# Kernel optimization log

Hardware: AMD Instinct MI355X
Metric: run time of the kernel (lower is better)

The kernel has to match this reference:

```python
import jax, jax.numpy as jnp
import numpy as np

DIM = 1024
N_HEADS = 16
HEAD_DIM = DIM // N_HEADS
HIDDEN = 4 * DIM
B, T = 4, 2048
EPS = 1e-5


def setup_inputs() -> dict:
    key = jax.random.key(0)
    ks = jax.random.split(key, 12)
    s = lambda fan_in: 1.0 / np.sqrt(fan_in)
    return {
        "x": jax.random.normal(ks[0], (B, T, DIM), jnp.float32),
        "ln1_g": jnp.ones((DIM,), jnp.float32),
        "ln1_b": jnp.zeros((DIM,), jnp.float32),
        "qkv_w": jax.random.normal(ks[1], (DIM, 3 * DIM), jnp.float32) * s(DIM),
        "qkv_b": jnp.zeros((3 * DIM,), jnp.float32),
        "proj_w": jax.random.normal(ks[2], (DIM, DIM), jnp.float32) * s(DIM),
        "proj_b": jnp.zeros((DIM,), jnp.float32),
        "ln2_g": jnp.ones((DIM,), jnp.float32),
        "ln2_b": jnp.zeros((DIM,), jnp.float32),
        "ff1_w": jax.random.normal(ks[3], (DIM, HIDDEN), jnp.float32) * s(DIM),
        "ff1_b": jnp.zeros((HIDDEN,), jnp.float32),
        "ff2_w": jax.random.normal(ks[4], (HIDDEN, DIM), jnp.float32) * s(HIDDEN),
        "ff2_b": jnp.zeros((DIM,), jnp.float32),
    }


def _layernorm(x, g, b):
    mu = jnp.mean(x, axis=-1, keepdims=True)
    var = jnp.mean(jnp.square(x - mu), axis=-1, keepdims=True)
    return (x - mu) * jax.lax.rsqrt(var + EPS) * g + b


def _attn(x, qkv_w, qkv_b, proj_w, proj_b):
    Bx, Tx, C = x.shape
    qkv = (x @ qkv_w + qkv_b).reshape(Bx, Tx, 3, N_HEADS, HEAD_DIM)
    q, k, v = (qkv[:, :, i].transpose(0, 2, 1, 3) for i in range(3))  # [B,H,T,hd]
    att = jnp.einsum('bhqd,bhkd->bhqk', q, k) / np.sqrt(HEAD_DIM)
    causal = jnp.tril(jnp.ones((Tx, Tx), bool))
    att = jnp.where(causal, att, -jnp.inf)
    att = jax.nn.softmax(att, axis=-1)
    out = jnp.einsum('bhqk,bhkd->bhqd', att, v).transpose(0, 2, 1, 3).reshape(Bx, Tx, C)
    return out @ proj_w + proj_b


def reference(x, ln1_g, ln1_b, qkv_w, qkv_b, proj_w, proj_b,
              ln2_g, ln2_b, ff1_w, ff1_b, ff2_w, ff2_b):
    x = x + _attn(_layernorm(x, ln1_g, ln1_b), qkv_w, qkv_b, proj_w, proj_b)
    h = _layernorm(x, ln2_g, ln2_b)
    h = jax.nn.gelu(h @ ff1_w + ff1_b, approximate=False) @ ff2_w + ff2_b
    return x + h
```

## Files before the change

### kernel.cpp

```cpp
#include <hip/hip_runtime.h>
#include <hip/hip_bf16.h>
#include <math.h>

#define DIM 1024
#define NHEADS 16
#define HD 64
#define TT 2048
#define BB 4
#define MTOK (BB*TT)
#define HID 4096

typedef __attribute__((ext_vector_type(8))) short bf16x8;
typedef __attribute__((ext_vector_type(4))) float f32x4;
typedef unsigned short u16;
typedef unsigned int u32;

__device__ inline u16 f2b(float f){
  __hip_bfloat16 h = __float2bfloat16(f);
  return __builtin_bit_cast(u16, h);
}

__device__ inline u32 cvtpk(float lo, float hi_){
  u32 r;
  asm("v_cvt_pk_bf16_f32 %0, %1, %2" : "=v"(r) : "v"(lo), "v"(hi_));
  return r;
}

__device__ inline void load_lds16(const void* g, void* l){
  __builtin_amdgcn_global_load_lds(
      (const __attribute__((address_space(1))) void*)g,
      (__attribute__((address_space(3))) void*)l,
      16, 0, 0);
}

__global__ __launch_bounds__(256) void wconv_t(const float* __restrict__ W,
                                               u16* __restrict__ Wt, int K, int N){
  __shared__ float tl[32][33];
  const int k0 = blockIdx.x*32, n0 = blockIdx.y*32;
  const int tx = threadIdx.x & 31, ty = threadIdx.x >> 5;
  #pragma unroll
  for (int r=0;r<32;r+=8)
    tl[ty+r][tx] = W[(size_t)(k0+ty+r)*N + (n0+tx)];
  __syncthreads();
  #pragma unroll
  for (int r=0;r<32;r+=8)
    Wt[(size_t)(n0+ty+r)*K + (k0+tx)] = f2b(tl[tx][ty+r]);
}

__global__ __launch_bounds__(256) void ln_fwd(const float* __restrict__ x,
                                              const float* __restrict__ g,
                                              const float* __restrict__ bta,
                                              u16* __restrict__ out){
  const int row = blockIdx.x, t = threadIdx.x;
  const float4 v = ((const float4*)(x + (size_t)row*DIM))[t];
  float s  = v.x+v.y+v.z+v.w;
  float s2 = v.x*v.x+v.y*v.y+v.z*v.z+v.w*v.w;
  #pragma unroll
  for (int m=1;m<64;m<<=1){ s += __shfl_xor(s,m); s2 += __shfl_xor(s2,m); }
  __shared__ float red[8];
  if ((t&63)==0){ red[t>>6]=s; red[4+(t>>6)]=s2; }
  __syncthreads();
  s  = red[0]+red[1]+red[2]+red[3];
  s2 = red[4]+red[5]+red[6]+red[7];
  const float mu = s*(1.0f/DIM);
  const float rstd = rsqrtf(s2*(1.0f/DIM) - mu*mu + 1e-5f);
  const float4 gv = ((const float4*)g)[t];
  const float4 bv = ((const float4*)bta)[t];
  ushort4 ov;
  ov.x = f2b((v.x-mu)*rstd*gv.x + bv.x);
  ov.y = f2b((v.y-mu)*rstd*gv.y + bv.y);
  ov.z = f2b((v.z-mu)*rstd*gv.z + bv.z);
  ov.w = f2b((v.w-mu)*rstd*gv.w + bv.w);
  ((ushort4*)out)[(size_t)row*(DIM/4) + t] = ov;
}

template<int EPI>
__global__ __launch_bounds__(256) void gemm_bt(
    const u16* __restrict__ A, const u16* __restrict__ Bt,
    const float* __restrict__ bias, const float* __restrict__ resid,
    float* __restrict__ outf, u16* __restrict__ outh,
    u16* __restrict__ qo, u16* __restrict__ ko, u16* __restrict__ vo,
    int M, int N, int K)
{
  __shared__ __align__(16) u16 smem[16384];
  u16* As = smem;
  u16* Bs = smem + 8192;
  u16* Ct = smem;
  const int t = threadIdx.x, wv = t>>6, ln = t&63;
  const int nbx = gridDim.x, nwg = nbx*gridDim.y;
  const int bid = blockIdx.y*nbx + blockIdx.x;
  const int cpx = nwg>>3;
  const int wid = (bid&7)*cpx + (bid>>3);
  const int m0 = (wid/nbx)*128, n0 = (wid%nbx)*128;
  const int wr = wv>>1, wc = wv&1;
  const int hi = ln>>4, lr = hi*4, lc = ln&15;
  f32x4 acc[4][4] = {};

  int rdoff[2];
  #pragma unroll
  for (int kk=0; kk<2; kk++)
    rdoff[kk] = ((kk*4 + hi) ^ (lc&7)) << 3;

  for (int kt=0; kt<K; kt+=64){
    #pragma unroll
    for (int j=0;j<4;j++){
      const int chunk = j*256 + t;
      const int row = chunk>>3;
      const int cS  = (chunk&7) ^ (row&7);
      load_lds16(A  + (size_t)(m0+row)*K + kt + cS*8, (char*)As + chunk*16);
      load_lds16(Bt + (size_t)(n0+row)*K + kt + cS*8, (char*)Bs + chunk*16);
    }
    asm volatile("s_waitcnt vmcnt(0)" ::: "memory");
    __syncthreads();
    bf16x8 af[4][2], bfr[4][2];
    #pragma unroll
    for (int mi=0;mi<4;mi++){
      const int rbase = (wr*64 + mi*16 + lc) << 6;
      af[mi][0] = *(const bf16x8*)&As[rbase + rdoff[0]];
      af[mi][1] = *(const bf16x8*)&As[rbase + rdoff[1]];
    }
    #pragma unroll
    for (int ni=0;ni<4;ni++){
      const int rbase = (wc*64 + ni*16 + lc) << 6;
      bfr[ni][0] = *(const bf16x8*)&Bs[rbase + rdoff[0]];
      bfr[ni][1] = *(const bf16x8*)&Bs[rbase + rdoff[1]];
    }
    #pragma unroll
    for (int kk=0;kk<2;kk++)
      #pragma unroll
      for (int mi=0;mi<4;mi++)
        #pragma unroll
        for (int ni=0;ni<4;ni++)
          acc[mi][ni] = __builtin_amdgcn_mfma_f32_16x16x32_bf16(af[mi][kk], bfr[ni][kk], acc[mi][ni], 0,0,0);
    __syncthreads();
  }

  if constexpr (EPI==1 || EPI==3){
    #pragma unroll
    for (int ni=0;ni<4;ni++){
      const int gn = n0 + wc*64 + ni*16 + lc;
      const float bv = bias[gn];
      #pragma unroll
      for (int mi=0;mi<4;mi++){
        const int gmb = m0 + wr*64 + mi*16 + lr;
        f32x4 a = acc[mi][ni];
        #pragma unroll
        for (int i=0;i<4;i++){
          const size_t idx = (size_t)(gmb+i)*DIM + gn;
          outf[idx] = a[i] + bv + resid[idx];
        }
      }
    }
  } else {
    const int part = (EPI==0) ? (n0>>10) : 0;
    __syncthreads();
    #pragma unroll
    for (int ni=0;ni<4;ni++){
      const int gn = n0 + wc*64 + ni*16 + lc;
      const float bv = bias[gn];
      const int cl = wc*64 + ni*16 + lc;
      #pragma unroll
      for (int mi=0;mi<4;mi++){
        f32x4 a = acc[mi][ni];
        #pragma unroll
        for (int i=0;i<4;i++){
          const int rl = wr*64 + mi*16 + lr + i;
          float val = a[i] + bv;
          if constexpr (EPI==2){
            const float xx = val*val;
            const float w  = val * fmaf(xx, 0.10294322f, 2.30220781f);
            const float y  = exp2f(w);
            const float r_ = __builtin_amdgcn_rcpf(1.0f + y);
            val = val - val*r_;
          }
          int r = rl, c = cl;
          if (EPI==0 && part==2){ r = cl; c = rl; }
          const int chunk = c>>3;
          const int csw = (chunk&8) | ((chunk ^ (r&7)) & 7);
          Ct[(r<<7) + (csw<<3) + (c&7)] = f2b(val);
        }
      }
    }
    __syncthreads();
    const int cid = t & 7, rsub = t >> 3;
    const int bb = m0>>11, tok0b = m0&2047;
    const int h0 = (EPI==0) ? ((n0&1023)>>6) : 0;
    #pragma unroll
    for (int pass=0; pass<4; ++pass){
      const int rr = pass*32 + rsub;
      #pragma unroll
      for (int hh=0; hh<2; ++hh){
        const int chunk = hh*8 + cid;
        const int sw = (chunk&8) | ((chunk ^ (rr&7)) & 7);
        const bf16x8 vvv = *(const bf16x8*)&Ct[(rr<<7) + (sw<<3)];
        if constexpr (EPI==2){
          *(bf16x8*)&outh[(size_t)(m0+rr)*HID + n0 + chunk*8] = vvv;
        } else {
          if (part==2){
            const int head = h0 + (rr>>6), d = rr&63;
            *(bf16x8*)&vo[(((size_t)bb*NHEADS + head)*HD + d)*TT + tok0b + chunk*8] = vvv;
          } else {
            u16* dst = part ? ko : qo;
            const int head = h0 + hh;
            *(bf16x8*)&dst[(((size_t)bb*NHEADS + head)*TT + tok0b + rr)*HD + cid*8] = vvv;
          }
        }
      }
    }
  }
}

__global__ __launch_bounds__(512) void attn_fwd(
    const u16* __restrict__ qpt, const u16* __restrict__ kb, const u16* __restrict__ vtb,
    u16* __restrict__ o)
{
  __shared__ __align__(16) u16 Kd[2][64*64];
  __shared__ __align__(16) u16 Vd[2][64*64];
  const int t = threadIdx.x, wv = t>>6, ln = t&63;
  const int bid  = blockIdx.y*gridDim.x + blockIdx.x;
  const int orig = (bid&7)*128 + (bid>>3);
  const int bh   = orig>>4;
  const int qb   = 15 - (orig&15);
  const size_t base = (size_t)bh*TT*HD;
  const int hi = ln>>4, lc = ln&15;
  const int nt = 2*qb + 2;
  const int qbase = qb*128 + wv*16;
  const int qrow  = qbase + lc;

  const bf16x8 qf0 = *(const bf16x8*)(qpt + base + (size_t)qrow*HD + hi*8);
  const bf16x8 qf1 = *(const bf16x8*)(qpt + base + (size_t)qrow*HD + 32 + hi*8);
  f32x4 oacc[4] = {};
  f32x4 lsum = {0.f,0.f,0.f,0.f};
  float mrun = -1e30f;
  const float SCQ = 0.125f * 1.44269504f;
  bf16x8 ones;
  #pragma unroll
  for (int j=0;j<8;j++) ones[j] = (short)0x3F80;

  const int srow = t>>3;
  const int sch  = t&7;
  const int gch  = (sch ^ (srow&7))<<3;

  auto STAGE = [&](int nb, int kt){
    load_lds16(kb  + base + (size_t)(kt*64+srow)*HD + gch, &Kd[nb][srow*64 + sch*8]);
    load_lds16(vtb + base + (size_t)srow*TT + kt*64 + gch, &Vd[nb][srow*64 + sch*8]);
  };
  auto FRAG = [&](const u16* buf, int r, int ch)->bf16x8{
    return *(const bf16x8*)(buf + r*64 + ((ch ^ (r&7))<<3));
  };
  const int src0 = ((ln&16)<<1) + lc;
  const int src1 = src0 + 16;
  auto pick = [&](u32 w0, u32 w1, int src)->u32{
    const u32 a = (u32)__shfl((int)w0, src);
    const u32 b = (u32)__shfl((int)w1, src);
    return (hi<2) ? a : b;
  };

  int cur = 0;
  STAGE(0, 0);
  asm volatile("s_waitcnt vmcnt(0)" ::: "memory");
  __syncthreads();

  for (int kt=0; kt<nt; kt++){
    if (kt+1 < nt) STAGE(cur^1, kt+1);
    const u16* Kb = Kd[cur];
    const u16* Vb = Vd[cur];
    if (kt*64 <= qbase + 15){
      float sv[4][4];
      __builtin_amdgcn_s_setprio(1);
      #pragma unroll
      for (int cf=0;cf<4;cf++){
        const int r = cf*16 + lc;
        const bf16x8 kf0 = FRAG(Kb, r, hi);
        const bf16x8 kf1 = FRAG(Kb, r, hi+4);
        f32x4 z = {0.f,0.f,0.f,0.f};
        z = __builtin_amdgcn_mfma_f32_16x16x32_bf16(kf0, qf0, z, 0,0,0);
        z = __builtin_amdgcn_mfma_f32_16x16x32_bf16(kf1, qf1, z, 0,0,0);
        sv[cf][0]=z[0]; sv[cf][1]=z[1]; sv[cf][2]=z[2]; sv[cf][3]=z[3];
      }
      __builtin_amdgcn_s_setprio(0);
      float mx = -1e30f;
      if (kt*64 + 63 > qbase){
        #pragma unroll
        for (int cf=0;cf<4;cf++)
          #pragma unroll
          for (int i=0;i<4;i++){
            const int kvg = kt*64 + cf*16 + 4*hi + i;
            float s_ = sv[cf][i]*SCQ;
            s_ = (kvg > qrow) ? -1e30f : s_;
            sv[cf][i] = s_;
            mx = fmaxf(mx, s_);
          }
      } else {
        #pragma unroll
        for (int cf=0;cf<4;cf++)
          #pragma unroll
          for (int i=0;i<4;i++){
            const float s_ = sv[cf][i]*SCQ;
            sv[cf][i] = s_;
            mx = fmaxf(mx, s_);
          }
      }
      mx = fmaxf(mx, __shfl_xor(mx, 16));
      mx = fmaxf(mx, __shfl_xor(mx, 32));
      if (__any(mx > mrun + 11.0f)){
        const float mnew = fmaxf(mrun, mx);
        const float sc = exp2f(mrun - mnew);
        mrun = mnew;
        const float s0 = __shfl(sc, 4*hi+0);
        const float s1 = __shfl(sc, 4*hi+1);
        const float s2 = __shfl(sc, 4*hi+2);
        const float s3 = __shfl(sc, 4*hi+3);
        #pragma unroll
        for (int df=0;df<4;df++){
          oacc[df][0] *= s0; oacc[df][1] *= s1;
          oacc[df][2] *= s2; oacc[df][3] *= s3;
        }
        lsum[0] *= s0; lsum[1] *= s1; lsum[2] *= s2; lsum[3] *= s3;
      }
      u32 W[4][2];
      #pragma unroll
      for (int cf=0;cf<4;cf++){
        const float e0 = exp2f(sv[cf][0] - mrun);
        const float e1 = exp2f(sv[cf][1] - mrun);
        const float e2 = exp2f(sv[cf][2] - mrun);
        const float e3 = exp2f(sv[cf][3] - mrun);
        W[cf][0] = cvtpk(e0, e1);
        W[cf][1] = cvtpk(e2, e3);
      }
      uint4 uA, uB;
      uA.x = pick(W[0][0], W[1][0], src0);
      uA.y = pick(W[0][1], W[1][1], src0);
      uA.z = pick(W[0][0], W[1][0], src1);
      uA.w = pick(W[0][1], W[1][1], src1);
      uB.x = pick(W[2][0], W[3][0], src0);
      uB.y = pick(W[2][1], W[3][1], src0);
      uB.z = pick(W[2][0], W[3][0], src1);
      uB.w = pick(W[2][1], W[3][1], src1);
      const bf16x8 paA = __builtin_bit_cast(bf16x8, uA);
      const bf16x8 paB = __builtin_bit_cast(bf16x8, uB);
      __builtin_amdgcn_s_setprio(1);
      #pragma unroll
      for (int df=0;df<4;df++){
        const bf16x8 v0 = FRAG(Vb, df*16+lc, hi);
        const bf16x8 v1 = FRAG(Vb, df*16+lc, hi+4);
        oacc[df] = __builtin_amdgcn_mfma_f32_16x16x32_bf16(paA, v0, oacc[df], 0,0,0);
        oacc[df] = __builtin_amdgcn_mfma_f32_16x16x32_bf16(paB, v1, oacc[df], 0,0,0);
      }
      lsum = __builtin_amdgcn_mfma_f32_16x16x32_bf16(paA, ones, lsum, 0,0,0);
      lsum = __builtin_amdgcn_mfma_f32_16x16x32_bf16(paB, ones, lsum, 0,0,0);
      __builtin_amdgcn_s_setprio(0);
    }
    asm volatile("s_waitcnt vmcnt(0)" ::: "memory");
    __syncthreads();
    cur ^= 1;
  }

  const int b = bh>>4, h = bh&15;
  const float inv[4] = {1.0f/lsum[0], 1.0f/lsum[1], 1.0f/lsum[2], 1.0f/lsum[3]};
  const int qg0 = qbase + 4*hi;
  #pragma unroll
  for (int i=0;i<4;i++){
    const size_t rowb = ((size_t)b*TT + (size_t)(qg0 + i))*DIM + h*HD;
    #pragma unroll
    for (int df=0;df<4;df++)
      o[rowb + df*16 + lc] = f2b(oacc[df][i]*inv[i]);
  }
}

extern "C" void kernel_launch(void* const* d_in, const int* in_sizes, int n_in,
                              void* d_out, int out_size, void* d_ws, size_t ws_size,
                              hipStream_t stream){
  (void)in_sizes; (void)n_in; (void)out_size; (void)ws_size;
  const float* x     = (const float*)d_in[0];
  const float* ln1g  = (const float*)d_in[1];
  const float* ln1b  = (const float*)d_in[2];
  const float* qkvw  = (const float*)d_in[3];
  const float* qkvb  = (const float*)d_in[4];
  const float* projw = (const float*)d_in[5];
  const float* projb = (const float*)d_in[6];
  const float* ln2g  = (const float*)d_in[7];
  const float* ln2b  = (const float*)d_in[8];
  const float* ff1w  = (const float*)d_in[9];
  const float* ff1b  = (const float*)d_in[10];
  const float* ff2w  = (const float*)d_in[11];
  const float* ff2b  = (const float*)d_in[12];
  float* out = (float*)d_out;

  char* ws = (char*)d_ws;
  size_t off = 0;
  auto alloc = [&](size_t n){ char* p = ws + off; off += (n + 255) & ~(size_t)255; return p; };
  u16* wqkvt  = (u16*)alloc((size_t)3072*1024*2);
  u16* wprojt = (u16*)alloc((size_t)1024*1024*2);
  u16* wff1t  = (u16*)alloc((size_t)4096*1024*2);
  u16* wff2t  = (u16*)alloc((size_t)1024*4096*2);
  u16* h1     = (u16*)alloc((size_t)MTOK*DIM*2);
  u16* qbuf   = (u16*)alloc((size_t)MTOK*DIM*2);
  u16* kbuf   = (u16*)alloc((size_t)MTOK*DIM*2);
  u16* vbuf   = (u16*)alloc((size_t)MTOK*DIM*2);
  u16* aout   = (u16*)alloc((size_t)MTOK*DIM*2);
  float* x2   = (float*)alloc((size_t)MTOK*DIM*4);
  u16* h2     = (u16*)alloc((size_t)MTOK*DIM*2);
  u16* act    = (u16*)alloc((size_t)MTOK*HID*2);

  wconv_t<<<dim3(1024/32, 3072/32), 256, 0, stream>>>(qkvw, wqkvt, 1024, 3072);
  wconv_t<<<dim3(1024/32, 1024/32), 256, 0, stream>>>(projw, wprojt, 1024, 1024);
  wconv_t<<<dim3(1024/32, 4096/32), 256, 0, stream>>>(ff1w, wff1t, 1024, 4096);
  wconv_t<<<dim3(4096/32, 1024/32), 256, 0, stream>>>(ff2w, wff2t, 4096, 1024);

  ln_fwd<<<MTOK, 256, 0, stream>>>(x, ln1g, ln1b, h1);

  gemm_bt<0><<<dim3(3072/128, MTOK/128), 256, 0, stream>>>(
      h1, wqkvt, qkvb, nullptr, nullptr, nullptr, qbuf, kbuf, vbuf, MTOK, 3072, 1024);

  attn_fwd<<<dim3(TT/128, BB*NHEADS), 512, 0, stream>>>(qbuf, kbuf, vbuf, aout);

  gemm_bt<1><<<dim3(1024/128, MTOK/128), 256, 0, stream>>>(
      aout, wprojt, projb, x, x2, nullptr, nullptr, nullptr, nullptr, MTOK, 1024, 1024);

  ln_fwd<<<MTOK, 256, 0, stream>>>(x2, ln2g, ln2b, h2);

  gemm_bt<2><<<dim3(4096/128, MTOK/128), 256, 0, stream>>>(
      h2, wff1t, ff1b, nullptr, nullptr, act, nullptr, nullptr, nullptr, MTOK, HID, 1024);

  gemm_bt<3><<<dim3(1024/128, MTOK/128), 256, 0, stream>>>(
      act, wff2t, ff2b, x2, out, nullptr, nullptr, nullptr, nullptr, MTOK, DIM, HID);
}
```

Measured before the change: 464.2 us.

## Add 256x256-tile double-buffered GEMM for QKV and FF1 projections

Introduces a new 512-thread GEMM kernel with 256x256 output tiles, 128KB of dynamic LDS, a double-buffered K pipeline that interleaves global-to-LDS staging with MFMA work, and an LDS-staged epilogue for the QKV scatter and the GELU output. It is used for the QKV and FF1 GEMMs when the large shared-memory attribute can be set, and falls back to the old kernel otherwise. The larger tiles raise arithmetic intensity and cut redundant operand loads. In exchange the grid has fewer workgroups, so occupancy is lower, and register pressure rises from the 8x4 accumulator array per wave.

```diff
diff --git a/kernel.cpp b/kernel.cpp
--- a/kernel.cpp
+++ b/kernel.cpp
@@ -72,6 +72,148 @@
   ov.z = f2b((v.z-mu)*rstd*gv.z + bv.z);
   ov.w = f2b((v.w-mu)*rstd*gv.w + bv.w);
   ((ushort4*)out)[(size_t)row*(DIM/4) + t] = ov;
+}
+
+template<int EPI>
+__global__ __launch_bounds__(512, 2) void gemm256(
+    const u16* __restrict__ A, const u16* __restrict__ Bt,
+    const float* __restrict__ bias, u16* __restrict__ outh,
+    u16* __restrict__ qo, u16* __restrict__ ko, u16* __restrict__ vo,
+    int K)
+{
+  extern __shared__ __align__(16) u16 smem[];
+  u16* Ct = smem;
+  const int t = threadIdx.x, wv = t>>6, ln = t&63;
+  const int nbx = gridDim.x, nwg = nbx*gridDim.y;
+  const int bid = blockIdx.y*nbx + blockIdx.x;
+  const int cpx = nwg>>3;
+  const int wid = (bid&7)*cpx + (bid>>3);
+  const int m0 = (wid/nbx)*256, n0 = (wid%nbx)*256;
+  const int wr = wv>>2, wc = wv&3;
+  const int hi = ln>>4, lc = ln&15;
+  f32x4 acc[8][4] = {};
+
+  auto STAGE = [&](int buf, int kt, int which, int kk){
+    const u16* src = which ? Bt : A;
+    const int org = which ? n0 : m0;
+    u16* dst = smem + buf*32768 + which*16384 + kk*8192;
+    #pragma unroll
+    for (int j=0;j<2;j++){
+      const int id = j*512 + t;
+      const int row = id>>2, c = id&3;
+      load_lds16(src + (size_t)(org+row)*K + kt*64 + kk*32 + ((c^(row&3))<<3),
+                 (char*)(dst + id*8));
+    }
+  };
+  auto AFRAG = [&](int buf, int kk, int r)->bf16x8{
+    return *(const bf16x8*)(smem + buf*32768 + kk*8192 + r*32 + ((hi^(r&3))<<3));
+  };
+  auto BFRAG = [&](int buf, int kk, int r)->bf16x8{
+    return *(const bf16x8*)(smem + buf*32768 + 16384 + kk*8192 + r*32 + ((hi^(r&3))<<3));
+  };
+
+  const int nkt = K>>6;
+  STAGE(0,0,0,0); STAGE(0,0,1,0); STAGE(0,0,0,1); STAGE(0,0,1,1);
+  asm volatile("s_waitcnt vmcnt(4)" ::: "memory");
+  __builtin_amdgcn_s_barrier();
+
+  int cur = 0;
+  for (int tt=0; tt<nkt; ++tt){
+    const int nxt = cur^1;
+    const bool st = (tt+1) < nkt;
+    bf16x8 bfr[4];
+    #pragma unroll
+    for (int p=0;p<4;p++){
+      const int kk = p>>1, mh = p&1;
+      if (mh==0){
+        #pragma unroll
+        for (int ni=0;ni<4;ni++)
+          bfr[ni] = BFRAG(cur, kk, wc*64 + ni*16 + lc);
+      }
+      bf16x8 af[4];
+      #pragma unroll
+      for (int mi=0;mi<4;mi++)
+        af[mi] = AFRAG(cur, kk, wr*128 + (mh*4+mi)*16 + lc);
+      if (st) STAGE(nxt, tt+1, p&1, p>>1);
+      __builtin_amdgcn_s_setprio(1);
+      #pragma unroll
+      for (int mi=0;mi<4;mi++)
+        #pragma unroll
+        for (int ni=0;ni<4;ni++)
+          acc[mh*4+mi][ni] = __builtin_amdgcn_mfma_f32_16x16x32_bf16(af[mi], bfr[ni], acc[mh*4+mi][ni], 0,0,0);
+      __builtin_amdgcn_s_setprio(0);
+      if (p==1 || p==3){
+        if (st) asm volatile("s_waitcnt vmcnt(4)" ::: "memory");
+        else    asm volatile("s_waitcnt vmcnt(0)" ::: "memory");
+        __builtin_amdgcn_s_barrier();
+      }
+    }
+    cur = nxt;
+  }
+
+  const int bb = m0>>11;
+  #pragma unroll
+  for (int h=0;h<2;h++){
+    #pragma unroll
+    for (int ch=0;ch<2;ch++){
+      const int part = (EPI==0) ? ((n0 + ch*128)>>10) : 0;
+      const int h0 = ((n0 + ch*128)&1023)>>6;
+      __syncthreads();
+      if (wr==h && (wc>>1)==ch){
+        #pragma unroll
+        for (int ni=0;ni<4;ni++){
+          const int gn = n0 + wc*64 + ni*16 + lc;
+          const float bv = bias[gn];
+          const int cl = (wc&1)*64 + ni*16 + lc;
+          #pragma unroll
+          for (int mi=0;mi<8;mi++){
+            f32x4 a = acc[mi][ni];
+            #pragma unroll
+            for (int i=0;i<4;i++){
+              const int rl = mi*16 + hi*4 + i;
+              float val = a[i] + bv;
+              if constexpr (EPI==2){
+                const float xx = val*val;
+                const float w  = val * fmaf(xx, 0.10294322f, 2.30220781f);
+                const float y  = exp2f(w);
+                const float r_ = __builtin_amdgcn_rcpf(1.0f + y);
+                val = val - val*r_;
+              }
+              int r = rl, c = cl;
+              if (EPI==0 && part==2){ r = cl; c = rl; }
+              const int chunk = c>>3;
+              const int csw = (chunk&8) | ((chunk ^ (r&7)) & 7);
+              Ct[(r<<7) + (csw<<3) + (c&7)] = f2b(val);
+            }
+          }
+        }
+      }
+      __syncthreads();
+      const int cid = t&7, rsub = t>>3;
+      const int tok0b = (m0&2047) + h*128;
+      #pragma unroll
+      for (int p2=0;p2<2;p2++){
+        const int rr = p2*64 + rsub;
+        #pragma unroll
+        for (int hh=0;hh<2;hh++){
+          const int chunk = hh*8 + cid;
+          const int sw = (chunk&8) | ((chunk ^ (rr&7)) & 7);
+          const bf16x8 vvv = *(const bf16x8*)&Ct[(rr<<7) + (sw<<3)];
+          if constexpr (EPI==2){
+            *(bf16x8*)&outh[(size_t)(m0 + h*128 + rr)*HID + n0 + ch*128 + chunk*8] = vvv;
+          } else {
+            if (part==2){
+              const int head = h0 + (rr>>6), d = rr&63;
+              *(bf16x8*)&vo[(((size_t)bb*NHEADS + head)*HD + d)*TT + tok0b + chunk*8] = vvv;
+            } else {
+              u16* dst = part ? ko : qo;
+              *(bf16x8*)&dst[(((size_t)bb*NHEADS + h0 + hh)*TT + tok0b + rr)*HD + cid*8] = vvv;
+            }
+          }
+        }
+      }
+    }
+  }
 }
 
 template<int EPI>
@@ -403,6 +545,12 @@
   u16* h2     = (u16*)alloc((size_t)MTOK*DIM*2);
   u16* act    = (u16*)alloc((size_t)MTOK*HID*2);
 
+  hipError_t eA = hipFuncSetAttribute(reinterpret_cast<const void*>(&gemm256<0>),
+                                      hipFuncAttributeMaxDynamicSharedMemorySize, 131072);
+  hipError_t eB = hipFuncSetAttribute(reinterpret_cast<const void*>(&gemm256<2>),
+                                      hipFuncAttributeMaxDynamicSharedMemorySize, 131072);
+  const bool big = (eA == hipSuccess) && (eB == hipSuccess);
+
   wconv_t<<<dim3(1024/32, 3072/32), 256, 0, stream>>>(qkvw, wqkvt, 1024, 3072);
   wconv_t<<<dim3(1024/32, 1024/32), 256, 0, stream>>>(projw, wprojt, 1024, 1024);
   wconv_t<<<dim3(1024/32, 4096/32), 256, 0, stream>>>(ff1w, wff1t, 1024, 4096);
@@ -410,8 +558,12 @@
 
   ln_fwd<<<MTOK, 256, 0, stream>>>(x, ln1g, ln1b, h1);
 
-  gemm_bt<0><<<dim3(3072/128, MTOK/128), 256, 0, stream>>>(
-      h1, wqkvt, qkvb, nullptr, nullptr, nullptr, qbuf, kbuf, vbuf, MTOK, 3072, 1024);
+  if (big)
+    gemm256<0><<<dim3(3072/256, MTOK/256), 512, 131072, stream>>>(
+        h1, wqkvt, qkvb, nullptr, qbuf, kbuf, vbuf, 1024);
+  else
+    gemm_bt<0><<<dim3(3072/128, MTOK/128), 256, 0, stream>>>(
+        h1, wqkvt, qkvb, nullptr, nullptr, nullptr, qbuf, kbuf, vbuf, MTOK, 3072, 1024);
 
   attn_fwd<<<dim3(TT/128, BB*NHEADS), 512, 0, stream>>>(qbuf, kbuf, vbuf, aout);
 
@@ -420,8 +572,12 @@
 
   ln_fwd<<<MTOK, 256, 0, stream>>>(x2, ln2g, ln2b, h2);
 
-  gemm_bt<2><<<dim3(4096/128, MTOK/128), 256, 0, stream>>>(
-      h2, wff1t, ff1b, nullptr, nullptr, act, nullptr, nullptr, nullptr, MTOK, HID, 1024);
+  if (big)
+    gemm256<2><<<dim3(4096/256, MTOK/256), 512, 131072, stream>>>(
+        h2, wff1t, ff1b, act, nullptr, nullptr, nullptr, 1024);
+  else
+    gemm_bt<2><<<dim3(4096/128, MTOK/128), 256, 0, stream>>>(
+        h2, wff1t, ff1b, nullptr, nullptr, act, nullptr, nullptr, nullptr, MTOK, HID, 1024);
 
   gemm_bt<3><<<dim3(1024/128, MTOK/128), 256, 0, stream>>>(
       act, wff2t, ff2b, x2, out, nullptr, nullptr, nullptr, nullptr, MTOK, DIM, HID);
```

Result: slower. 514.7 us (+10.9%).

## Pair complementary causal query blocks per attention workgroup to balance work

Applied to the files above, without the earlier changes.

Each attention workgroup now processes two query blocks, qp and 15-qp, over a single shared K/V stream. The goal is to balance causal work across workgroups and reuse each staged K/V tile for both query strips. In exchange the grid halves to 512 workgroups and register pressure roughly doubles because two sets of accumulators are live, which may lower occupancy.

```diff
diff --git a/kernel.cpp b/kernel.cpp
--- a/kernel.cpp
+++ b/kernel.cpp
@@ -218,20 +218,23 @@
   __shared__ __align__(16) u16 Vd[2][64*64];
   const int t = threadIdx.x, wv = t>>6, ln = t&63;
   const int bid  = blockIdx.y*gridDim.x + blockIdx.x;
-  const int orig = (bid&7)*128 + (bid>>3);
-  const int bh   = orig>>4;
-  const int qb   = 15 - (orig&15);
+  const int orig = (bid&7)*64 + (bid>>3);
+  const int bh   = orig>>3;
+  const int qp   = orig&7;
+  const int qbA  = qp, qbB = 15-qp;
   const size_t base = (size_t)bh*TT*HD;
   const int hi = ln>>4, lc = ln&15;
-  const int nt = 2*qb + 2;
-  const int qbase = qb*128 + wv*16;
-  const int qrow  = qbase + lc;
-
-  const bf16x8 qf0 = *(const bf16x8*)(qpt + base + (size_t)qrow*HD + hi*8);
-  const bf16x8 qf1 = *(const bf16x8*)(qpt + base + (size_t)qrow*HD + 32 + hi*8);
-  f32x4 oacc[4] = {};
-  f32x4 lsum = {0.f,0.f,0.f,0.f};
-  float mrun = -1e30f;
+  const int ntA = 2*qbA + 2, ntB = 2*qbB + 2;
+  const int qbaseA = qbA*128 + wv*16, qrowA = qbaseA + lc;
+  const int qbaseB = qbB*128 + wv*16, qrowB = qbaseB + lc;
+
+  const bf16x8 qfA0 = *(const bf16x8*)(qpt + base + (size_t)qrowA*HD + hi*8);
+  const bf16x8 qfA1 = *(const bf16x8*)(qpt + base + (size_t)qrowA*HD + 32 + hi*8);
+  const bf16x8 qfB0 = *(const bf16x8*)(qpt + base + (size_t)qrowB*HD + hi*8);
+  const bf16x8 qfB1 = *(const bf16x8*)(qpt + base + (size_t)qrowB*HD + 32 + hi*8);
+  f32x4 oaccA[4] = {}, oaccB[4] = {};
+  f32x4 lsumA = {0.f,0.f,0.f,0.f}, lsumB = {0.f,0.f,0.f,0.f};
+  float mrunA = -1e30f, mrunB = -1e30f;
   const float SCQ = 0.125f * 1.44269504f;
   bf16x8 ones;
   #pragma unroll
@@ -256,115 +259,136 @@
     return (hi<2) ? a : b;
   };
 
+  auto strip_tile = [&](int kt, const u16* Kb, const u16* Vb,
+                        const bf16x8& qf0, const bf16x8& qf1,
+                        int qbase, int qrow,
+                        f32x4* oacc, f32x4& lsum, float& mrun){
+    if (kt*64 > qbase + 15) return;
+    float sv[4][4];
+    __builtin_amdgcn_s_setprio(1);
+    #pragma unroll
+    for (int cf=0;cf<4;cf++){
+      const int r = cf*16 + lc;
+      const bf16x8 kf0 = FRAG(Kb, r, hi);
+      const bf16x8 kf1 = FRAG(Kb, r, hi+4);
+      f32x4 z = {0.f,0.f,0.f,0.f};
+      z = __builtin_amdgcn_mfma_f32_16x16x32_bf16(kf0, qf0, z, 0,0,0);
+      z = __builtin_amdgcn_mfma_f32_16x16x32_bf16(kf1, qf1, z, 0,0,0);
+      sv[cf][0]=z[0]; sv[cf][1]=z[1]; sv[cf][2]=z[2]; sv[cf][3]=z[3];
+    }
+    __builtin_amdgcn_s_setprio(0);
+    float mx = -1e30f;
+    if (kt*64 + 63 > qbase){
+      #pragma unroll
+      for (int cf=0;cf<4;cf++)
+        #pragma unroll
+        for (int i=0;i<4;i++){
+          const int kvg = kt*64 + cf*16 + 4*hi + i;
+          float s_ = sv[cf][i]*SCQ;
+          s_ = (kvg > qrow) ? -1e30f : s_;
+          sv[cf][i] = s_;
+          mx = fmaxf(mx, s_);
+        }
+    } else {
+      #pragma unroll
+      for (int cf=0;cf<4;cf++)
+        #pragma unroll
+        for (int i=0;i<4;i++){
+          const float s_ = sv[cf][i]*SCQ;
+          sv[cf][i] = s_;
+          mx = fmaxf(mx, s_);
+        }
+    }
+    mx = fmaxf(mx, __shfl_xor(mx, 16));
+    mx = fmaxf(mx, __shfl_xor(mx, 32));
+    if (__any(mx > mrun + 11.0f)){
+      const float mnew = fmaxf(mrun, mx);
+      const float sc = exp2f(mrun - mnew);
+      mrun = mnew;
+      const float s0 = __shfl(sc, 4*hi+0);
+      const float s1 = __shfl(sc, 4*hi+1);
+      const float s2 = __shfl(sc, 4*hi+2);
+      const float s3 = __shfl(sc, 4*hi+3);
+      #pragma unroll
+      for (int df=0;df<4;df++){
+        oacc[df][0] *= s0; oacc[df][1] *= s1;
+        oacc[df][2] *= s2; oacc[df][3] *= s3;
+      }
+      lsum[0] *= s0; lsum[1] *= s1; lsum[2] *= s2; lsum[3] *= s3;
+    }
+    u32 W[4][2];
+    #pragma unroll
+    for (int cf=0;cf<4;cf++){
+      const float e0 = exp2f(sv[cf][0] - mrun);
+      const float e1 = exp2f(sv[cf][1] - mrun);
+      const float e2 = exp2f(sv[cf][2] - mrun);
+      const float e3 = exp2f(sv[cf][3] - mrun);
+      W[cf][0] = cvtpk(e0, e1);
+      W[cf][1] = cvtpk(e2, e3);
+    }
+    uint4 uA, uB;
+    uA.x = pick(W[0][0], W[1][0], src0);
+    uA.y = pick(W[0][1], W[1][1], src0);
+    uA.z = pick(W[0][0], W[1][0], src1);
+    uA.w = pick(W[0][1], W[1][1], src1);
+    uB.x = pick(W[2][0], W[3][0], src0);
+    uB.y = pick(W[2][1], W[3][1], src0);
+    uB.z = pick(W[2][0], W[3][0], src1);
+    uB.w = pick(W[2][1], W[3][1], src1);
+    const bf16x8 paA = __builtin_bit_cast(bf16x8, uA);
+    const bf16x8 paB = __builtin_bit_cast(bf16x8, uB);
+    __builtin_amdgcn_s_setprio(1);
+    #pragma unroll
+    for (int df=0;df<4;df++){
+      const bf16x8 v0 = FRAG(Vb, df*16+lc, hi);
+      const bf16x8 v1 = FRAG(Vb, df*16+lc, hi+4);
+      oacc[df] = __builtin_amdgcn_mfma_f32_16x16x32_bf16(paA, v0, oacc[df], 0,0,0);
+      oacc[df] = __builtin_amdgcn_mfma_f32_16x16x32_bf16(paB, v1, oacc[df], 0,0,0);
+    }
+    lsum = __builtin_amdgcn_mfma_f32_16x16x32_bf16(paA, ones, lsum, 0,0,0);
+    lsum = __builtin_amdgcn_mfma_f32_16x16x32_bf16(paB, ones, lsum, 0,0,0);
+    __builtin_amdgcn_s_setprio(0);
+  };
+
   int cur = 0;
   STAGE(0, 0);
   asm volatile("s_waitcnt vmcnt(0)" ::: "memory");
   __syncthreads();
 
-  for (int kt=0; kt<nt; kt++){
-    if (kt+1 < nt) STAGE(cur^1, kt+1);
+  for (int kt=0; kt<ntB; kt++){
+    if (kt+1 < ntB) STAGE(cur^1, kt+1);
     const u16* Kb = Kd[cur];
     const u16* Vb = Vd[cur];
-    if (kt*64 <= qbase + 15){
-      float sv[4][4];
-      __builtin_amdgcn_s_setprio(1);
-      #pragma unroll
-      for (int cf=0;cf<4;cf++){
-        const int r = cf*16 + lc;
-        const bf16x8 kf0 = FRAG(Kb, r, hi);
-        const bf16x8 kf1 = FRAG(Kb, r, hi+4);
-        f32x4 z = {0.f,0.f,0.f,0.f};
-        z = __builtin_amdgcn_mfma_f32_16x16x32_bf16(kf0, qf0, z, 0,0,0);
-        z = __builtin_amdgcn_mfma_f32_16x16x32_bf16(kf1, qf1, z, 0,0,0);
-        sv[cf][0]=z[0]; sv[cf][1]=z[1]; sv[cf][2]=z[2]; sv[cf][3]=z[3];
-      }
-      __builtin_amdgcn_s_setprio(0);
-      float mx = -1e30f;
-      if (kt*64 + 63 > qbase){
-        #pragma unroll
-        for (int cf=0;cf<4;cf++)
-          #pragma unroll
-          for (int i=0;i<4;i++){
-            const int kvg = kt*64 + cf*16 + 4*hi + i;
-            float s_ = sv[cf][i]*SCQ;
-            s_ = (kvg > qrow) ? -1e30f : s_;
-            sv[cf][i] = s_;
-            mx = fmaxf(mx, s_);
-          }
-      } else {
-        #pragma unroll
-        for (int cf=0;cf<4;cf++)
-          #pragma unroll
-          for (int i=0;i<4;i++){
-            const float s_ = sv[cf][i]*SCQ;
-            sv[cf][i] = s_;
-            mx = fmaxf(mx, s_);
-          }
-      }
-      mx = fmaxf(mx, __shfl_xor(mx, 16));
-      mx = fmaxf(mx, __shfl_xor(mx, 32));
-      if (__any(mx > mrun + 11.0f)){
-        const float mnew = fmaxf(mrun, mx);
-        const float sc = exp2f(mrun - mnew);
-        mrun = mnew;
-        const float s0 = __shfl(sc, 4*hi+0);
-        const float s1 = __shfl(sc, 4*hi+1);
-        const float s2 = __shfl(sc, 4*hi+2);
-        const float s3 = __shfl(sc, 4*hi+3);
-        #pragma unroll
-        for (int df=0;df<4;df++){
-          oacc[df][0] *= s0; oacc[df][1] *= s1;
-          oacc[df][2] *= s2; oacc[df][3] *= s3;
-        }
-        lsum[0] *= s0; lsum[1] *= s1; lsum[2] *= s2; lsum[3] *= s3;
-      }
-      u32 W[4][2];
-      #pragma unroll
-      for (int cf=0;cf<4;cf++){
-        const float e0 = exp2f(sv[cf][0] - mrun);
-        const float e1 = exp2f(sv[cf][1] - mrun);
-        const float e2 = exp2f(sv[cf][2] - mrun);
-        const float e3 = exp2f(sv[cf][3] - mrun);
-        W[cf][0] = cvtpk(e0, e1);
-        W[cf][1] = cvtpk(e2, e3);
-      }
-      uint4 uA, uB;
-      uA.x = pick(W[0][0], W[1][0], src0);
-      uA.y = pick(W[0][1], W[1][1], src0);
-      uA.z = pick(W[0][0], W[1][0], src1);
-      uA.w = pick(W[0][1], W[1][1], src1);
-      uB.x = pick(W[2][0], W[3][0], src0);
-      uB.y = pick(W[2][1], W[3][1], src0);
-      uB.z = pick(W[2][0], W[3][0], src1);
-      uB.w = pick(W[2][1], W[3][1], src1);
-      const bf16x8 paA = __builtin_bit_cast(bf16x8, uA);
-      const bf16x8 paB = __builtin_bit_cast(bf16x8, uB);
-      __builtin_amdgcn_s_setprio(1);
-      #pragma unroll
-      for (int df=0;df<4;df++){
-        const bf16x8 v0 = FRAG(Vb, df*16+lc, hi);
-        const bf16x8 v1 = FRAG(Vb, df*16+lc, hi+4);
-        oacc[df] = __builtin_amdgcn_mfma_f32_16x16x32_bf16(paA, v0, oacc[df], 0,0,0);
-        oacc[df] = __builtin_amdgcn_mfma_f32_16x16x32_bf16(paB, v1, oacc[df], 0,0,0);
-      }
-      lsum = __builtin_amdgcn_mfma_f32_16x16x32_bf16(paA, ones, lsum, 0,0,0);
-      lsum = __builtin_amdgcn_mfma_f32_16x16x32_bf16(paB, ones, lsum, 0,0,0);
-      __builtin_amdgcn_s_setprio(0);
-    }
+    strip_tile(kt, Kb, Vb, qfB0, qfB1, qbaseB, qrowB, oaccB, lsumB, mrunB);
+    if (kt < ntA)
+      strip_tile(kt, Kb, Vb, qfA0, qfA1, qbaseA, qrowA, oaccA, lsumA, mrunA);
     asm volatile("s_waitcnt vmcnt(0)" ::: "memory");
     __syncthreads();
     cur ^= 1;
   }
 
   const int b = bh>>4, h = bh&15;
-  const float inv[4] = {1.0f/lsum[0], 1.0f/lsum[1], 1.0f/lsum[2], 1.0f/lsum[3]};
-  const int qg0 = qbase + 4*hi;
-  #pragma unroll
-  for (int i=0;i<4;i++){
-    const size_t rowb = ((size_t)b*TT + (size_t)(qg0 + i))*DIM + h*HD;
-    #pragma unroll
-    for (int df=0;df<4;df++)
-      o[rowb + df*16 + lc] = f2b(oacc[df][i]*inv[i]);
+  {
+    const float inv[4] = {1.0f/lsumA[0], 1.0f/lsumA[1], 1.0f/lsumA[2], 1.0f/lsumA[3]};
+    const int qg0 = qbaseA + 4*hi;
+    #pragma unroll
+    for (int i=0;i<4;i++){
+      const size_t rowb = ((size_t)b*TT + (size_t)(qg0 + i))*DIM + h*HD;
+      #pragma unroll
+      for (int df=0;df<4;df++)
+        o[rowb + df*16 + lc] = f2b(oaccA[df][i]*inv[i]);
+    }
+  }
+  {
+    const float inv[4] = {1.0f/lsumB[0], 1.0f/lsumB[1], 1.0f/lsumB[2], 1.0f/lsumB[3]};
+    const int qg0 = qbaseB + 4*hi;
+    #pragma unroll
+    for (int i=0;i<4;i++){
+      const size_t rowb = ((size_t)b*TT + (size_t)(qg0 + i))*DIM + h*HD;
+      #pragma unroll
+      for (int df=0;df<4;df++)
+        o[rowb + df*16 + lc] = f2b(oaccB[df][i]*inv[i]);
+    }
   }
 }
 
@@ -413,7 +437,7 @@
   gemm_bt<0><<<dim3(3072/128, MTOK/128), 256, 0, stream>>>(
       h1, wqkvt, qkvb, nullptr, nullptr, nullptr, qbuf, kbuf, vbuf, MTOK, 3072, 1024);
 
-  attn_fwd<<<dim3(TT/128, BB*NHEADS), 512, 0, stream>>>(qbuf, kbuf, vbuf, aout);
+  attn_fwd<<<dim3(8, BB*NHEADS), 512, 0, stream>>>(qbuf, kbuf, vbuf, aout);
 
   gemm_bt<1><<<dim3(1024/128, MTOK/128), 256, 0, stream>>>(
       aout, wprojt, projb, x, x2, nullptr, nullptr, nullptr, nullptr, MTOK, 1024, 1024);
```

Result: faster. 436.9 us (-5.9%).
